# Optimization experiments

Measured on AMD Instinct MI355X. Metric: run time of the kernel, lower is better.

The kernel has to match this reference:

```python
import jax, jax.numpy as jnp
import numpy as np

NUM_INPUTS = 24
FACTOR = 16
VOCAB = 1_000_000
BATCH = 8192
PAIRS = NUM_INPUTS * (NUM_INPUTS - 1) // 2  # 276
HIDDEN = 64


def setup_inputs() -> dict:
    key = jax.random.key(0)
    ks = jax.random.split(key, 8)
    inputs = jax.random.randint(ks[0], (BATCH, NUM_INPUTS), 0, VOCAB)
    s = 0.01
    w = jax.random.normal(ks[1], (VOCAB, 1), dtype=jnp.float32) * s
    v = jax.random.normal(ks[2], (VOCAB, FACTOR), dtype=jnp.float32) * s
    b = jnp.zeros((1,), dtype=jnp.float32)
    W1 = jax.random.normal(ks[3], (PAIRS, 2 * FACTOR, HIDDEN), dtype=jnp.float32) * s
    b1 = jnp.zeros((PAIRS, HIDDEN), dtype=jnp.float32)
    W2 = jax.random.normal(ks[4], (PAIRS, HIDDEN, 1), dtype=jnp.float32) * s
    b2 = jnp.zeros((PAIRS, 1), dtype=jnp.float32)
    return {"inputs": inputs, "w": w, "v": v, "b": b,
            "W1": W1, "b1": b1, "W2": W2, "b2": b2}


def reference(inputs, w, v, b, W1, b1, W2, b2):
    # pair index lists (i < j) -- static
    ii, jj = np.triu_indices(NUM_INPUTS, k=1)
    ii = jnp.asarray(ii)
    jj = jnp.asarray(jj)

    # linear term: sum of 1-dim embeddings over fields
    xw = w[inputs]                      # [B, n, 1]
    l = jnp.sum(xw, axis=(1, 2))        # [B]

    # pairwise concat of factor embeddings
    xv = v[inputs]                      # [B, n, f]
    prods = jnp.concatenate([xv[:, ii, :], xv[:, jj, :]], axis=-1)  # [B, P, 2f]
    prods = jnp.transpose(prods, (1, 0, 2))                         # [P, B, 2f]

    # per-pair stacked MLP: layer 0 relu, layer 1 identity
    h = jax.nn.relu(jnp.einsum('pbi,pio->pbo', prods, W1) + b1[:, None, :])  # [P, B, H]
    out = jnp.einsum('pbi,pio->pbo', h, W2) + b2[:, None, :]                  # [P, B, 1]

    # sum over concat of pair outputs == sum over pairs and last dim
    p = jnp.sum(out, axis=(0, 2))       # [B]

    logits = l + p + b[0]
    return jax.nn.sigmoid(logits)
```

## Files before the change

### kernel.cpp

```cpp
#include <hip/hip_runtime.h>
#include <hip/hip_bf16.h>
#include <math.h>

#define BATCH   8192
#define NFIELD  24
#define FAC     16
#define PAIRS   276
#define HID     64
#define PG      6
#define PPG     (PAIRS / PG)
#define NBB     (BATCH / 64)

typedef __attribute__((ext_vector_type(8))) __bf16 bf16x8;
typedef __attribute__((ext_vector_type(4))) float f32x4;

#define XVT_OFF   0
#define COMBO_OFF 6291456
#define PART_OFF  (COMBO_OFF + 1276416)
#define CONST_OFF (PART_OFF + 196608)

__global__ void prep_embed(const int* __restrict__ inputs,
                           const float* __restrict__ v,
                           __hip_bfloat16* __restrict__ xvT) {
    int t = blockIdx.x * 256 + threadIdx.x;
    int field = t >> 13;
    int b = t & 8191;
    int idx = inputs[b * NFIELD + field];
    const float4* src = (const float4*)(v + (long)idx * FAC);
    union { __hip_bfloat16 h[16]; uint4 u[2]; } tmp;
    float4 a0 = src[0], a1 = src[1], a2 = src[2], a3 = src[3];
    tmp.h[0]  = __float2bfloat16(a0.x); tmp.h[1]  = __float2bfloat16(a0.y);
    tmp.h[2]  = __float2bfloat16(a0.z); tmp.h[3]  = __float2bfloat16(a0.w);
    tmp.h[4]  = __float2bfloat16(a1.x); tmp.h[5]  = __float2bfloat16(a1.y);
    tmp.h[6]  = __float2bfloat16(a1.z); tmp.h[7]  = __float2bfloat16(a1.w);
    tmp.h[8]  = __float2bfloat16(a2.x); tmp.h[9]  = __float2bfloat16(a2.y);
    tmp.h[10] = __float2bfloat16(a2.z); tmp.h[11] = __float2bfloat16(a2.w);
    tmp.h[12] = __float2bfloat16(a3.x); tmp.h[13] = __float2bfloat16(a3.y);
    tmp.h[14] = __float2bfloat16(a3.z); tmp.h[15] = __float2bfloat16(a3.w);
    int bb = b >> 6, row = b & 63;
    __hip_bfloat16* base = xvT + (long)bb * 24576 + field * 1024 + row * 8;
    *(uint4*)base         = tmp.u[0];
    *(uint4*)(base + 512) = tmp.u[1];
}

__global__ void prep_w(const float* __restrict__ W1,
                       const float* __restrict__ W2,
                       const float* __restrict__ b1,
                       const float* __restrict__ b2,
                       const float* __restrict__ bsc,
                       char* __restrict__ combo,
                       float* __restrict__ consts) {
    __shared__ float red[256];
    int t = blockIdx.x * 256 + threadIdx.x;
    int p = t >> 6;
    int L = t & 63;
    int q = L >> 4, c = L & 15;
    char* base = combo + (long)p * 4608;
    union { __hip_bfloat16 h[8]; uint4 u; } buf;
#pragma unroll
    for (int tt = 0; tt < 4; ++tt) {
#pragma unroll
        for (int jj = 0; jj < 8; ++jj)
            buf.h[jj] = __float2bfloat16(W1[p * 2048 + (q * 8 + jj) * 64 + tt * 16 + c]);
        *(uint4*)(base + 512 + tt * 1024 + L * 16) = buf.u;
    }
    if (L < 16) {
        float4 bv = {b1[p * 64 + L], b1[p * 64 + 16 + L], b1[p * 64 + 32 + L], b1[p * 64 + 48 + L]};
        *(float4*)(base + L * 16) = bv;
        float4 wv = {W2[p * 64 + L], W2[p * 64 + 16 + L], W2[p * 64 + 32 + L], W2[p * 64 + 48 + L]};
        *(float4*)(base + 256 + L * 16) = wv;
    }
    if (blockIdx.x == 1) {
        uint4 z = {0, 0, 0, 0};
        for (int k = threadIdx.x; k < 288; k += 256)
            *(uint4*)(combo + (long)PAIRS * 4608 + k * 16) = z;
    }
    if (blockIdx.x == 0) {
        float s = 0.f;
        for (int k = threadIdx.x; k < PAIRS; k += 256) s += b2[k];
        red[threadIdx.x] = s;
        __syncthreads();
        for (int off = 128; off > 0; off >>= 1) {
            if (threadIdx.x < off) red[threadIdx.x] += red[threadIdx.x + off];
            __syncthreads();
        }
        if (threadIdx.x == 0) consts[0] = red[0] + bsc[0];
    }
}

__global__ __launch_bounds__(256, 4) void ffm_main(
        const __hip_bfloat16* __restrict__ xvT,
        const char* __restrict__ combo,
        float* __restrict__ partial) {
    __shared__ __align__(16) __hip_bfloat16 xv_s[24 * 1088];

    int tid  = threadIdx.x;
    int bb   = blockIdx.x & (NBB - 1);
    int pg   = blockIdx.x >> 7;
    int lane = tid & 63;
    int wave = tid >> 6;
    int col  = lane & 15;
    int quad = lane >> 4;

    {
        const uint4* src = (const uint4*)(xvT + (long)bb * 24576);
#pragma unroll
        for (int it = 0; it < 12; ++it) {
            int ch = tid + it * 256;
            *(uint4*)(xv_s + ch * 8 + (ch >> 6) * 32) = src[ch];
        }
    }
    __syncthreads();

    int p0 = pg * PPG;
    int i = 0, rem = p0;
    while (rem >= NFIELD - 1 - i) { rem -= NFIELD - 1 - i; ++i; }
    int j = i + 1 + rem;

    const int arow = (quad & 1) * 544 + (wave * 16 + col) * 8;
    const int mcol = col * 16;
    const char* wp = combo + (long)p0 * 4608;

    float4 mb1 = *(const float4*)(wp + mcol);
    float4 mw2 = *(const float4*)(wp + 256 + mcol);
    bf16x8 f0 = *(const bf16x8*)(wp + 512 + lane * 16);
    bf16x8 f1 = *(const bf16x8*)(wp + 1536 + lane * 16);
    bf16x8 f2 = *(const bf16x8*)(wp + 2560 + lane * 16);
    bf16x8 f3 = *(const bf16x8*)(wp + 3584 + lane * 16);

    float a0 = 0.f, a1 = 0.f, a2 = 0.f, a3 = 0.f;

#pragma unroll 2
    for (int it = 0; it < PPG; ++it) {
        const char* wn = wp + 4608;
        float4 nb1 = *(const float4*)(wn + mcol);
        float4 nw2 = *(const float4*)(wn + 256 + mcol);
        bf16x8 nf0 = *(const bf16x8*)(wn + 512 + lane * 16);
        bf16x8 nf1 = *(const bf16x8*)(wn + 1536 + lane * 16);
        bf16x8 nf2 = *(const bf16x8*)(wn + 2560 + lane * 16);
        bf16x8 nf3 = *(const bf16x8*)(wn + 3584 + lane * 16);

        int fso = (quad < 2) ? i * 1088 : j * 1088;
        bf16x8 af = *(const bf16x8*)(xv_s + fso + arow);

        f32x4 c0 = {mb1.x, mb1.x, mb1.x, mb1.x};
        f32x4 c1 = {mb1.y, mb1.y, mb1.y, mb1.y};
        f32x4 c2 = {mb1.z, mb1.z, mb1.z, mb1.z};
        f32x4 c3 = {mb1.w, mb1.w, mb1.w, mb1.w};
        c0 = __builtin_amdgcn_mfma_f32_16x16x32_bf16(af, f0, c0, 0, 0, 0);
        c1 = __builtin_amdgcn_mfma_f32_16x16x32_bf16(af, f1, c1, 0, 0, 0);
        c2 = __builtin_amdgcn_mfma_f32_16x16x32_bf16(af, f2, c2, 0, 0, 0);
        c3 = __builtin_amdgcn_mfma_f32_16x16x32_bf16(af, f3, c3, 0, 0, 0);

        a0 = fmaf(fmaxf(c0[0], 0.f), mw2.x, a0);
        a1 = fmaf(fmaxf(c0[1], 0.f), mw2.x, a1);
        a2 = fmaf(fmaxf(c0[2], 0.f), mw2.x, a2);
        a3 = fmaf(fmaxf(c0[3], 0.f), mw2.x, a3);
        a0 = fmaf(fmaxf(c1[0], 0.f), mw2.y, a0);
        a1 = fmaf(fmaxf(c1[1], 0.f), mw2.y, a1);
        a2 = fmaf(fmaxf(c1[2], 0.f), mw2.y, a2);
        a3 = fmaf(fmaxf(c1[3], 0.f), mw2.y, a3);
        a0 = fmaf(fmaxf(c2[0], 0.f), mw2.z, a0);
        a1 = fmaf(fmaxf(c2[1], 0.f), mw2.z, a1);
        a2 = fmaf(fmaxf(c2[2], 0.f), mw2.z, a2);
        a3 = fmaf(fmaxf(c2[3], 0.f), mw2.z, a3);
        a0 = fmaf(fmaxf(c3[0], 0.f), mw2.w, a0);
        a1 = fmaf(fmaxf(c3[1], 0.f), mw2.w, a1);
        a2 = fmaf(fmaxf(c3[2], 0.f), mw2.w, a2);
        a3 = fmaf(fmaxf(c3[3], 0.f), mw2.w, a3);

        mb1 = nb1; mw2 = nw2; f0 = nf0; f1 = nf1; f2 = nf2; f3 = nf3;
        wp = wn;
        ++j;
        if (j == NFIELD) { ++i; j = i + 1; }
    }

#pragma unroll
    for (int m = 1; m < 16; m <<= 1) {
        a0 += __shfl_xor(a0, m, 64);
        a1 += __shfl_xor(a1, m, 64);
        a2 += __shfl_xor(a2, m, 64);
        a3 += __shfl_xor(a3, m, 64);
    }
    if (col == 0) {
        f32x4 o; o[0] = a0; o[1] = a1; o[2] = a2; o[3] = a3;
        *(f32x4*)&partial[pg * BATCH + bb * 64 + wave * 16 + quad * 4] = o;
    }
}

__global__ void finalize(const int* __restrict__ inputs,
                         const float* __restrict__ w,
                         const float* __restrict__ consts,
                         const float* __restrict__ partial,
                         float* __restrict__ out) {
    int bidx = blockIdx.x * 256 + threadIdx.x;
    const int4* ip = (const int4*)(inputs + bidx * NFIELD);
    float l = 0.f;
#pragma unroll
    for (int q = 0; q < 6; ++q) {
        int4 v4 = ip[q];
        l += w[v4.x] + w[v4.y] + w[v4.z] + w[v4.w];
    }
    float s = l + consts[0];
#pragma unroll
    for (int g = 0; g < PG; ++g) s += partial[g * BATCH + bidx];
    out[bidx] = 1.0f / (1.0f + expf(-s));
}

extern "C" void kernel_launch(void* const* d_in, const int* in_sizes, int n_in,
                              void* d_out, int out_size, void* d_ws, size_t ws_size,
                              hipStream_t stream) {
    const int*   inputs = (const int*)d_in[0];
    const float* w      = (const float*)d_in[1];
    const float* v      = (const float*)d_in[2];
    const float* bsc    = (const float*)d_in[3];
    const float* W1     = (const float*)d_in[4];
    const float* b1     = (const float*)d_in[5];
    const float* W2     = (const float*)d_in[6];
    const float* b2     = (const float*)d_in[7];
    float* out = (float*)d_out;

    char* ws = (char*)d_ws;
    __hip_bfloat16* xvT = (__hip_bfloat16*)(ws + XVT_OFF);
    char*  combo  = ws + COMBO_OFF;
    float* partial = (float*)(ws + PART_OFF);
    float* consts  = (float*)(ws + CONST_OFF);

    prep_embed<<<BATCH * NFIELD / 256, 256, 0, stream>>>(inputs, v, xvT);
    prep_w<<<PAIRS * 64 / 256, 256, 0, stream>>>(W1, W2, b1, b2, bsc, combo, consts);
    ffm_main<<<NBB * PG, 256, 0, stream>>>(xvT, combo, partial);
    finalize<<<BATCH / 256, 256, 0, stream>>>(inputs, w, consts, partial, out);
}
```

Measured before the change: 157.1 us.

## Merge prep kernels and share LDS embedding tile across two pair groups

The two preprocessing kernels become one launch that splits work by block index, which removes a kernel launch. The main kernel now uses 512-thread blocks in which two halves handle different pair groups over the same staged 64-row embedding tile, halving the global-to-LDS reload of embeddings. The weight prefetch becomes an explicit double-buffered ping-pong of two pair slots, and the zero padding at the end of combo is enlarged so the deeper prefetch does not read past it. More registers per thread and fewer blocks may reduce occupancy and latency hiding.

New measurement: 162.3 us. +3.3%, slower.

```diff
diff --git a/kernel.cpp b/kernel.cpp
--- a/kernel.cpp
+++ b/kernel.cpp
@@ -16,79 +16,122 @@
 
 #define XVT_OFF   0
 #define COMBO_OFF 6291456
-#define PART_OFF  (COMBO_OFF + 1276416)
+#define PART_OFF  (COMBO_OFF + 1281024)
 #define CONST_OFF (PART_OFF + 196608)
 
-__global__ void prep_embed(const int* __restrict__ inputs,
-                           const float* __restrict__ v,
-                           __hip_bfloat16* __restrict__ xvT) {
-    int t = blockIdx.x * 256 + threadIdx.x;
-    int field = t >> 13;
-    int b = t & 8191;
-    int idx = inputs[b * NFIELD + field];
-    const float4* src = (const float4*)(v + (long)idx * FAC);
-    union { __hip_bfloat16 h[16]; uint4 u[2]; } tmp;
-    float4 a0 = src[0], a1 = src[1], a2 = src[2], a3 = src[3];
-    tmp.h[0]  = __float2bfloat16(a0.x); tmp.h[1]  = __float2bfloat16(a0.y);
-    tmp.h[2]  = __float2bfloat16(a0.z); tmp.h[3]  = __float2bfloat16(a0.w);
-    tmp.h[4]  = __float2bfloat16(a1.x); tmp.h[5]  = __float2bfloat16(a1.y);
-    tmp.h[6]  = __float2bfloat16(a1.z); tmp.h[7]  = __float2bfloat16(a1.w);
-    tmp.h[8]  = __float2bfloat16(a2.x); tmp.h[9]  = __float2bfloat16(a2.y);
-    tmp.h[10] = __float2bfloat16(a2.z); tmp.h[11] = __float2bfloat16(a2.w);
-    tmp.h[12] = __float2bfloat16(a3.x); tmp.h[13] = __float2bfloat16(a3.y);
-    tmp.h[14] = __float2bfloat16(a3.z); tmp.h[15] = __float2bfloat16(a3.w);
-    int bb = b >> 6, row = b & 63;
-    __hip_bfloat16* base = xvT + (long)bb * 24576 + field * 1024 + row * 8;
-    *(uint4*)base         = tmp.u[0];
-    *(uint4*)(base + 512) = tmp.u[1];
-}
-
-__global__ void prep_w(const float* __restrict__ W1,
-                       const float* __restrict__ W2,
-                       const float* __restrict__ b1,
-                       const float* __restrict__ b2,
-                       const float* __restrict__ bsc,
-                       char* __restrict__ combo,
-                       float* __restrict__ consts) {
+__global__ void prep_all(const int* __restrict__ inputs,
+                         const float* __restrict__ v,
+                         const float* __restrict__ W1,
+                         const float* __restrict__ W2,
+                         const float* __restrict__ b1,
+                         const float* __restrict__ b2,
+                         const float* __restrict__ bsc,
+                         __hip_bfloat16* __restrict__ xvT,
+                         char* __restrict__ combo,
+                         float* __restrict__ consts) {
     __shared__ float red[256];
-    int t = blockIdx.x * 256 + threadIdx.x;
-    int p = t >> 6;
-    int L = t & 63;
-    int q = L >> 4, c = L & 15;
-    char* base = combo + (long)p * 4608;
-    union { __hip_bfloat16 h[8]; uint4 u; } buf;
-#pragma unroll
-    for (int tt = 0; tt < 4; ++tt) {
-#pragma unroll
-        for (int jj = 0; jj < 8; ++jj)
-            buf.h[jj] = __float2bfloat16(W1[p * 2048 + (q * 8 + jj) * 64 + tt * 16 + c]);
-        *(uint4*)(base + 512 + tt * 1024 + L * 16) = buf.u;
-    }
-    if (L < 16) {
-        float4 bv = {b1[p * 64 + L], b1[p * 64 + 16 + L], b1[p * 64 + 32 + L], b1[p * 64 + 48 + L]};
-        *(float4*)(base + L * 16) = bv;
-        float4 wv = {W2[p * 64 + L], W2[p * 64 + 16 + L], W2[p * 64 + 32 + L], W2[p * 64 + 48 + L]};
-        *(float4*)(base + 256 + L * 16) = wv;
-    }
-    if (blockIdx.x == 1) {
-        uint4 z = {0, 0, 0, 0};
-        for (int k = threadIdx.x; k < 288; k += 256)
-            *(uint4*)(combo + (long)PAIRS * 4608 + k * 16) = z;
-    }
-    if (blockIdx.x == 0) {
-        float s = 0.f;
-        for (int k = threadIdx.x; k < PAIRS; k += 256) s += b2[k];
-        red[threadIdx.x] = s;
-        __syncthreads();
-        for (int off = 128; off > 0; off >>= 1) {
-            if (threadIdx.x < off) red[threadIdx.x] += red[threadIdx.x + off];
+    int blk = blockIdx.x;
+    if (blk < 768) {
+        int t = blk * 256 + threadIdx.x;
+        int field = t >> 13;
+        int b = t & 8191;
+        int idx = inputs[b * NFIELD + field];
+        const float4* src = (const float4*)(v + (long)idx * FAC);
+        union { __hip_bfloat16 h[16]; uint4 u[2]; } tmp;
+        float4 a0 = src[0], a1 = src[1], a2 = src[2], a3 = src[3];
+        tmp.h[0]  = __float2bfloat16(a0.x); tmp.h[1]  = __float2bfloat16(a0.y);
+        tmp.h[2]  = __float2bfloat16(a0.z); tmp.h[3]  = __float2bfloat16(a0.w);
+        tmp.h[4]  = __float2bfloat16(a1.x); tmp.h[5]  = __float2bfloat16(a1.y);
+        tmp.h[6]  = __float2bfloat16(a1.z); tmp.h[7]  = __float2bfloat16(a1.w);
+        tmp.h[8]  = __float2bfloat16(a2.x); tmp.h[9]  = __float2bfloat16(a2.y);
+        tmp.h[10] = __float2bfloat16(a2.z); tmp.h[11] = __float2bfloat16(a2.w);
+        tmp.h[12] = __float2bfloat16(a3.x); tmp.h[13] = __float2bfloat16(a3.y);
+        tmp.h[14] = __float2bfloat16(a3.z); tmp.h[15] = __float2bfloat16(a3.w);
+        int bb = b >> 6, row = b & 63;
+        __hip_bfloat16* base = xvT + (long)bb * 24576 + field * 1024 + row * 8;
+        *(uint4*)base         = tmp.u[0];
+        *(uint4*)(base + 512) = tmp.u[1];
+    } else {
+        int wb = blk - 768;
+        int t = wb * 256 + threadIdx.x;
+        int p = t >> 6;
+        int L = t & 63;
+        int q = L >> 4, c = L & 15;
+        char* base = combo + (long)p * 4608;
+        union { __hip_bfloat16 h[8]; uint4 u; } buf;
+#pragma unroll
+        for (int tt = 0; tt < 4; ++tt) {
+#pragma unroll
+            for (int jj = 0; jj < 8; ++jj)
+                buf.h[jj] = __float2bfloat16(W1[p * 2048 + (q * 8 + jj) * 64 + tt * 16 + c]);
+            *(uint4*)(base + 512 + tt * 1024 + L * 16) = buf.u;
+        }
+        if (L < 16) {
+            float4 bv = {b1[p * 64 + L], b1[p * 64 + 16 + L], b1[p * 64 + 32 + L], b1[p * 64 + 48 + L]};
+            *(float4*)(base + L * 16) = bv;
+            float4 wv = {W2[p * 64 + L], W2[p * 64 + 16 + L], W2[p * 64 + 32 + L], W2[p * 64 + 48 + L]};
+            *(float4*)(base + 256 + L * 16) = wv;
+        }
+        if (wb == 1) {
+            uint4 z = {0, 0, 0, 0};
+            for (int k = threadIdx.x; k < 576; k += 256)
+                *(uint4*)(combo + (long)PAIRS * 4608 + k * 16) = z;
+        }
+        if (wb == 0) {
+            float s = 0.f;
+            for (int k = threadIdx.x; k < PAIRS; k += 256) s += b2[k];
+            red[threadIdx.x] = s;
             __syncthreads();
-        }
-        if (threadIdx.x == 0) consts[0] = red[0] + bsc[0];
-    }
-}
-
-__global__ __launch_bounds__(256, 4) void ffm_main(
+            for (int off = 128; off > 0; off >>= 1) {
+                if (threadIdx.x < off) red[threadIdx.x] += red[threadIdx.x + off];
+                __syncthreads();
+            }
+            if (threadIdx.x == 0) consts[0] = red[0] + bsc[0];
+        }
+    }
+}
+
+#define LOADSET(MB1, MW2, F0, F1, F2, F3, PTR)        \
+    MB1 = *(const float4*)((PTR) + mcol);             \
+    MW2 = *(const float4*)((PTR) + 256 + mcol);       \
+    F0  = *(const bf16x8*)((PTR) + 512  + l16);       \
+    F1  = *(const bf16x8*)((PTR) + 1536 + l16);       \
+    F2  = *(const bf16x8*)((PTR) + 2560 + l16);       \
+    F3  = *(const bf16x8*)((PTR) + 3584 + l16);
+
+#define COMPUTE(MB1, MW2, F0, F1, F2, F3)                                    \
+    {                                                                        \
+        int fso = ((quad < 2) ? i : j) * 1088;                               \
+        bf16x8 af = *(const bf16x8*)(xv_s + fso + arow);                     \
+        f32x4 c0 = {MB1.x, MB1.x, MB1.x, MB1.x};                             \
+        f32x4 c1 = {MB1.y, MB1.y, MB1.y, MB1.y};                             \
+        f32x4 c2 = {MB1.z, MB1.z, MB1.z, MB1.z};                             \
+        f32x4 c3 = {MB1.w, MB1.w, MB1.w, MB1.w};                             \
+        c0 = __builtin_amdgcn_mfma_f32_16x16x32_bf16(af, F0, c0, 0, 0, 0);   \
+        c1 = __builtin_amdgcn_mfma_f32_16x16x32_bf16(af, F1, c1, 0, 0, 0);   \
+        c2 = __builtin_amdgcn_mfma_f32_16x16x32_bf16(af, F2, c2, 0, 0, 0);   \
+        c3 = __builtin_amdgcn_mfma_f32_16x16x32_bf16(af, F3, c3, 0, 0, 0);   \
+        a0 = fmaf(fmaxf(c0[0], 0.f), MW2.x, a0);                             \
+        a1 = fmaf(fmaxf(c0[1], 0.f), MW2.x, a1);                             \
+        a2 = fmaf(fmaxf(c0[2], 0.f), MW2.x, a2);                             \
+        a3 = fmaf(fmaxf(c0[3], 0.f), MW2.x, a3);                             \
+        a0 = fmaf(fmaxf(c1[0], 0.f), MW2.y, a0);                             \
+        a1 = fmaf(fmaxf(c1[1], 0.f), MW2.y, a1);                             \
+        a2 = fmaf(fmaxf(c1[2], 0.f), MW2.y, a2);                             \
+        a3 = fmaf(fmaxf(c1[3], 0.f), MW2.y, a3);                             \
+        a0 = fmaf(fmaxf(c2[0], 0.f), MW2.z, a0);                             \
+        a1 = fmaf(fmaxf(c2[1], 0.f), MW2.z, a1);                             \
+        a2 = fmaf(fmaxf(c2[2], 0.f), MW2.z, a2);                             \
+        a3 = fmaf(fmaxf(c2[3], 0.f), MW2.z, a3);                             \
+        a0 = fmaf(fmaxf(c3[0], 0.f), MW2.w, a0);                             \
+        a1 = fmaf(fmaxf(c3[1], 0.f), MW2.w, a1);                             \
+        a2 = fmaf(fmaxf(c3[2], 0.f), MW2.w, a2);                             \
+        a3 = fmaf(fmaxf(c3[3], 0.f), MW2.w, a3);                             \
+        ++j;                                                                 \
+        if (j == NFIELD) { ++i; j = i + 1; }                                 \
+    }
+
+__global__ __launch_bounds__(512, 4) void ffm_main(
         const __hip_bfloat16* __restrict__ xvT,
         const char* __restrict__ combo,
         float* __restrict__ partial) {
@@ -96,83 +139,48 @@
 
     int tid  = threadIdx.x;
     int bb   = blockIdx.x & (NBB - 1);
-    int pg   = blockIdx.x >> 7;
+    int bkpg = blockIdx.x >> 7;
     int lane = tid & 63;
     int wave = tid >> 6;
     int col  = lane & 15;
     int quad = lane >> 4;
+    int h    = wave >> 2;
+    int r    = wave & 3;
 
     {
         const uint4* src = (const uint4*)(xvT + (long)bb * 24576);
 #pragma unroll
-        for (int it = 0; it < 12; ++it) {
-            int ch = tid + it * 256;
+        for (int it = 0; it < 6; ++it) {
+            int ch = tid + it * 512;
             *(uint4*)(xv_s + ch * 8 + (ch >> 6) * 32) = src[ch];
         }
     }
     __syncthreads();
 
+    int pg = bkpg * 2 + h;
     int p0 = pg * PPG;
     int i = 0, rem = p0;
     while (rem >= NFIELD - 1 - i) { rem -= NFIELD - 1 - i; ++i; }
     int j = i + 1 + rem;
 
-    const int arow = (quad & 1) * 544 + (wave * 16 + col) * 8;
+    const int arow = (quad & 1) * 544 + (r * 16 + col) * 8;
     const int mcol = col * 16;
+    const int l16  = lane * 16;
     const char* wp = combo + (long)p0 * 4608;
 
-    float4 mb1 = *(const float4*)(wp + mcol);
-    float4 mw2 = *(const float4*)(wp + 256 + mcol);
-    bf16x8 f0 = *(const bf16x8*)(wp + 512 + lane * 16);
-    bf16x8 f1 = *(const bf16x8*)(wp + 1536 + lane * 16);
-    bf16x8 f2 = *(const bf16x8*)(wp + 2560 + lane * 16);
-    bf16x8 f3 = *(const bf16x8*)(wp + 3584 + lane * 16);
+    float4 mb1a, mw2a, mb1b, mw2b;
+    bf16x8 fa0, fa1, fa2, fa3, fb0, fb1, fb2, fb3;
+    LOADSET(mb1a, mw2a, fa0, fa1, fa2, fa3, wp)
+    LOADSET(mb1b, mw2b, fb0, fb1, fb2, fb3, wp + 4608)
 
     float a0 = 0.f, a1 = 0.f, a2 = 0.f, a3 = 0.f;
 
-#pragma unroll 2
-    for (int it = 0; it < PPG; ++it) {
-        const char* wn = wp + 4608;
-        float4 nb1 = *(const float4*)(wn + mcol);
-        float4 nw2 = *(const float4*)(wn + 256 + mcol);
-        bf16x8 nf0 = *(const bf16x8*)(wn + 512 + lane * 16);
-        bf16x8 nf1 = *(const bf16x8*)(wn + 1536 + lane * 16);
-        bf16x8 nf2 = *(const bf16x8*)(wn + 2560 + lane * 16);
-        bf16x8 nf3 = *(const bf16x8*)(wn + 3584 + lane * 16);
-
-        int fso = (quad < 2) ? i * 1088 : j * 1088;
-        bf16x8 af = *(const bf16x8*)(xv_s + fso + arow);
-
-        f32x4 c0 = {mb1.x, mb1.x, mb1.x, mb1.x};
-        f32x4 c1 = {mb1.y, mb1.y, mb1.y, mb1.y};
-        f32x4 c2 = {mb1.z, mb1.z, mb1.z, mb1.z};
-        f32x4 c3 = {mb1.w, mb1.w, mb1.w, mb1.w};
-        c0 = __builtin_amdgcn_mfma_f32_16x16x32_bf16(af, f0, c0, 0, 0, 0);
-        c1 = __builtin_amdgcn_mfma_f32_16x16x32_bf16(af, f1, c1, 0, 0, 0);
-        c2 = __builtin_amdgcn_mfma_f32_16x16x32_bf16(af, f2, c2, 0, 0, 0);
-        c3 = __builtin_amdgcn_mfma_f32_16x16x32_bf16(af, f3, c3, 0, 0, 0);
-
-        a0 = fmaf(fmaxf(c0[0], 0.f), mw2.x, a0);
-        a1 = fmaf(fmaxf(c0[1], 0.f), mw2.x, a1);
-        a2 = fmaf(fmaxf(c0[2], 0.f), mw2.x, a2);
-        a3 = fmaf(fmaxf(c0[3], 0.f), mw2.x, a3);
-        a0 = fmaf(fmaxf(c1[0], 0.f), mw2.y, a0);
-        a1 = fmaf(fmaxf(c1[1], 0.f), mw2.y, a1);
-        a2 = fmaf(fmaxf(c1[2], 0.f), mw2.y, a2);
-        a3 = fmaf(fmaxf(c1[3], 0.f), mw2.y, a3);
-        a0 = fmaf(fmaxf(c2[0], 0.f), mw2.z, a0);
-        a1 = fmaf(fmaxf(c2[1], 0.f), mw2.z, a1);
-        a2 = fmaf(fmaxf(c2[2], 0.f), mw2.z, a2);
-        a3 = fmaf(fmaxf(c2[3], 0.f), mw2.z, a3);
-        a0 = fmaf(fmaxf(c3[0], 0.f), mw2.w, a0);
-        a1 = fmaf(fmaxf(c3[1], 0.f), mw2.w, a1);
-        a2 = fmaf(fmaxf(c3[2], 0.f), mw2.w, a2);
-        a3 = fmaf(fmaxf(c3[3], 0.f), mw2.w, a3);
-
-        mb1 = nb1; mw2 = nw2; f0 = nf0; f1 = nf1; f2 = nf2; f3 = nf3;
-        wp = wn;
-        ++j;
-        if (j == NFIELD) { ++i; j = i + 1; }
+    for (int k = 0; k < PPG; k += 2) {
+        COMPUTE(mb1a, mw2a, fa0, fa1, fa2, fa3)
+        LOADSET(mb1a, mw2a, fa0, fa1, fa2, fa3, wp + 2 * 4608)
+        COMPUTE(mb1b, mw2b, fb0, fb1, fb2, fb3)
+        LOADSET(mb1b, mw2b, fb0, fb1, fb2, fb3, wp + 3 * 4608)
+        wp += 2 * 4608;
     }
 
 #pragma unroll
@@ -184,7 +192,7 @@
     }
     if (col == 0) {
         f32x4 o; o[0] = a0; o[1] = a1; o[2] = a2; o[3] = a3;
-        *(f32x4*)&partial[pg * BATCH + bb * 64 + wave * 16 + quad * 4] = o;
+        *(f32x4*)&partial[pg * BATCH + bb * 64 + r * 16 + quad * 4] = o;
     }
 }
 
@@ -222,12 +230,11 @@
 
     char* ws = (char*)d_ws;
     __hip_bfloat16* xvT = (__hip_bfloat16*)(ws + XVT_OFF);
-    char*  combo  = ws + COMBO_OFF;
+    char*  combo   = ws + COMBO_OFF;
     float* partial = (float*)(ws + PART_OFF);
     float* consts  = (float*)(ws + CONST_OFF);
 
-    prep_embed<<<BATCH * NFIELD / 256, 256, 0, stream>>>(inputs, v, xvT);
-    prep_w<<<PAIRS * 64 / 256, 256, 0, stream>>>(W1, W2, b1, b2, bsc, combo, consts);
-    ffm_main<<<NBB * PG, 256, 0, stream>>>(xvT, combo, partial);
+    prep_all<<<768 + 69, 256, 0, stream>>>(inputs, v, W1, W2, b1, b2, bsc, xvT, combo, consts);
+    ffm_main<<<NBB * 3, 512, 0, stream>>>(xvT, combo, partial);
     finalize<<<BATCH / 256, 256, 0, stream>>>(inputs, w, consts, partial, out);
 }
```

## Give each wave a pair set over all 64 rows and merge prep kernels

Applied to the files above, without the earlier changes.

The main kernel now gives each wave its own set of 12 pairs and has it process all 64 batch rows of the tile. Each loaded weight fragment is reused across four MFMA row tiles instead of one, which cuts weight traffic per block. The pair space is split into 24 sets, the last of which does no work, so finalize now sums 24 partials instead of 6, and the partial buffer grows accordingly. The two prep kernels are also merged into a single launch to save one kernel launch. In exchange, each wave holds 16 accumulators, which raises register pressure.

After: 150.3 us. 1.05x faster.

```diff
diff --git a/kernel.cpp b/kernel.cpp
--- a/kernel.cpp
+++ b/kernel.cpp
@@ -7,8 +7,8 @@
 #define FAC     16
 #define PAIRS   276
 #define HID     64
-#define PG      6
-#define PPG     (PAIRS / PG)
+#define NSETS   24
+#define SETLEN  12
 #define NBB     (BATCH / 64)
 
 typedef __attribute__((ext_vector_type(8))) __bf16 bf16x8;
@@ -16,75 +16,78 @@
 
 #define XVT_OFF   0
 #define COMBO_OFF 6291456
-#define PART_OFF  (COMBO_OFF + 1276416)
-#define CONST_OFF (PART_OFF + 196608)
-
-__global__ void prep_embed(const int* __restrict__ inputs,
-                           const float* __restrict__ v,
-                           __hip_bfloat16* __restrict__ xvT) {
-    int t = blockIdx.x * 256 + threadIdx.x;
-    int field = t >> 13;
-    int b = t & 8191;
-    int idx = inputs[b * NFIELD + field];
-    const float4* src = (const float4*)(v + (long)idx * FAC);
-    union { __hip_bfloat16 h[16]; uint4 u[2]; } tmp;
-    float4 a0 = src[0], a1 = src[1], a2 = src[2], a3 = src[3];
-    tmp.h[0]  = __float2bfloat16(a0.x); tmp.h[1]  = __float2bfloat16(a0.y);
-    tmp.h[2]  = __float2bfloat16(a0.z); tmp.h[3]  = __float2bfloat16(a0.w);
-    tmp.h[4]  = __float2bfloat16(a1.x); tmp.h[5]  = __float2bfloat16(a1.y);
-    tmp.h[6]  = __float2bfloat16(a1.z); tmp.h[7]  = __float2bfloat16(a1.w);
-    tmp.h[8]  = __float2bfloat16(a2.x); tmp.h[9]  = __float2bfloat16(a2.y);
-    tmp.h[10] = __float2bfloat16(a2.z); tmp.h[11] = __float2bfloat16(a2.w);
-    tmp.h[12] = __float2bfloat16(a3.x); tmp.h[13] = __float2bfloat16(a3.y);
-    tmp.h[14] = __float2bfloat16(a3.z); tmp.h[15] = __float2bfloat16(a3.w);
-    int bb = b >> 6, row = b & 63;
-    __hip_bfloat16* base = xvT + (long)bb * 24576 + field * 1024 + row * 8;
-    *(uint4*)base         = tmp.u[0];
-    *(uint4*)(base + 512) = tmp.u[1];
-}
-
-__global__ void prep_w(const float* __restrict__ W1,
-                       const float* __restrict__ W2,
-                       const float* __restrict__ b1,
-                       const float* __restrict__ b2,
-                       const float* __restrict__ bsc,
-                       char* __restrict__ combo,
-                       float* __restrict__ consts) {
+#define PART_OFF  (COMBO_OFF + 1285632)
+#define CONST_OFF (PART_OFF + 786432)
+
+__global__ void prep_all(const int* __restrict__ inputs,
+                         const float* __restrict__ v,
+                         const float* __restrict__ W1,
+                         const float* __restrict__ W2,
+                         const float* __restrict__ b1,
+                         const float* __restrict__ b2,
+                         const float* __restrict__ bsc,
+                         __hip_bfloat16* __restrict__ xvT,
+                         char* __restrict__ combo,
+                         float* __restrict__ consts) {
     __shared__ float red[256];
-    int t = blockIdx.x * 256 + threadIdx.x;
-    int p = t >> 6;
-    int L = t & 63;
-    int q = L >> 4, c = L & 15;
-    char* base = combo + (long)p * 4608;
-    union { __hip_bfloat16 h[8]; uint4 u; } buf;
-#pragma unroll
-    for (int tt = 0; tt < 4; ++tt) {
-#pragma unroll
-        for (int jj = 0; jj < 8; ++jj)
-            buf.h[jj] = __float2bfloat16(W1[p * 2048 + (q * 8 + jj) * 64 + tt * 16 + c]);
-        *(uint4*)(base + 512 + tt * 1024 + L * 16) = buf.u;
-    }
-    if (L < 16) {
-        float4 bv = {b1[p * 64 + L], b1[p * 64 + 16 + L], b1[p * 64 + 32 + L], b1[p * 64 + 48 + L]};
-        *(float4*)(base + L * 16) = bv;
-        float4 wv = {W2[p * 64 + L], W2[p * 64 + 16 + L], W2[p * 64 + 32 + L], W2[p * 64 + 48 + L]};
-        *(float4*)(base + 256 + L * 16) = wv;
-    }
-    if (blockIdx.x == 1) {
-        uint4 z = {0, 0, 0, 0};
-        for (int k = threadIdx.x; k < 288; k += 256)
-            *(uint4*)(combo + (long)PAIRS * 4608 + k * 16) = z;
-    }
-    if (blockIdx.x == 0) {
-        float s = 0.f;
-        for (int k = threadIdx.x; k < PAIRS; k += 256) s += b2[k];
-        red[threadIdx.x] = s;
-        __syncthreads();
-        for (int off = 128; off > 0; off >>= 1) {
-            if (threadIdx.x < off) red[threadIdx.x] += red[threadIdx.x + off];
+    int blk = blockIdx.x;
+    if (blk < 768) {
+        int t = blk * 256 + threadIdx.x;
+        int field = t >> 13;
+        int b = t & 8191;
+        int idx = inputs[b * NFIELD + field];
+        const float4* src = (const float4*)(v + (long)idx * FAC);
+        union { __hip_bfloat16 h[16]; uint4 u[2]; } tmp;
+        float4 a0 = src[0], a1 = src[1], a2 = src[2], a3 = src[3];
+        tmp.h[0]  = __float2bfloat16(a0.x); tmp.h[1]  = __float2bfloat16(a0.y);
+        tmp.h[2]  = __float2bfloat16(a0.z); tmp.h[3]  = __float2bfloat16(a0.w);
+        tmp.h[4]  = __float2bfloat16(a1.x); tmp.h[5]  = __float2bfloat16(a1.y);
+        tmp.h[6]  = __float2bfloat16(a1.z); tmp.h[7]  = __float2bfloat16(a1.w);
+        tmp.h[8]  = __float2bfloat16(a2.x); tmp.h[9]  = __float2bfloat16(a2.y);
+        tmp.h[10] = __float2bfloat16(a2.z); tmp.h[11] = __float2bfloat16(a2.w);
+        tmp.h[12] = __float2bfloat16(a3.x); tmp.h[13] = __float2bfloat16(a3.y);
+        tmp.h[14] = __float2bfloat16(a3.z); tmp.h[15] = __float2bfloat16(a3.w);
+        int bb = b >> 6, row = b & 63;
+        __hip_bfloat16* base = xvT + (long)bb * 24576 + field * 1024 + row * 8;
+        *(uint4*)base         = tmp.u[0];
+        *(uint4*)(base + 512) = tmp.u[1];
+    } else {
+        int wb = blk - 768;
+        int t = wb * 256 + threadIdx.x;
+        int p = t >> 6;
+        int L = t & 63;
+        int q = L >> 4, c = L & 15;
+        char* base = combo + (long)p * 4608;
+        union { __hip_bfloat16 h[8]; uint4 u; } buf;
+#pragma unroll
+        for (int tt = 0; tt < 4; ++tt) {
+#pragma unroll
+            for (int jj = 0; jj < 8; ++jj)
+                buf.h[jj] = __float2bfloat16(W1[p * 2048 + (q * 8 + jj) * 64 + tt * 16 + c]);
+            *(uint4*)(base + 512 + tt * 1024 + L * 16) = buf.u;
+        }
+        if (L < 16) {
+            float4 bv = {b1[p * 64 + L], b1[p * 64 + 16 + L], b1[p * 64 + 32 + L], b1[p * 64 + 48 + L]};
+            *(float4*)(base + L * 16) = bv;
+            float4 wv = {W2[p * 64 + L], W2[p * 64 + 16 + L], W2[p * 64 + 32 + L], W2[p * 64 + 48 + L]};
+            *(float4*)(base + 256 + L * 16) = wv;
+        }
+        if (wb == 1) {
+            uint4 z = {0, 0, 0, 0};
+            for (int k = threadIdx.x; k < 864; k += 256)
+                *(uint4*)(combo + (long)PAIRS * 4608 + k * 16) = z;
+        }
+        if (wb == 0) {
+            float s = 0.f;
+            for (int k = threadIdx.x; k < PAIRS; k += 256) s += b2[k];
+            red[threadIdx.x] = s;
             __syncthreads();
-        }
-        if (threadIdx.x == 0) consts[0] = red[0] + bsc[0];
+            for (int off = 128; off > 0; off >>= 1) {
+                if (threadIdx.x < off) red[threadIdx.x] += red[threadIdx.x + off];
+                __syncthreads();
+            }
+            if (threadIdx.x == 0) consts[0] = red[0] + bsc[0];
+        }
     }
 }
 
@@ -112,79 +115,77 @@
     }
     __syncthreads();
 
-    int p0 = pg * PPG;
-    int i = 0, rem = p0;
-    while (rem >= NFIELD - 1 - i) { rem -= NFIELD - 1 - i; ++i; }
-    int j = i + 1 + rem;
-
-    const int arow = (quad & 1) * 544 + (wave * 16 + col) * 8;
-    const int mcol = col * 16;
-    const char* wp = combo + (long)p0 * 4608;
-
-    float4 mb1 = *(const float4*)(wp + mcol);
-    float4 mw2 = *(const float4*)(wp + 256 + mcol);
-    bf16x8 f0 = *(const bf16x8*)(wp + 512 + lane * 16);
-    bf16x8 f1 = *(const bf16x8*)(wp + 1536 + lane * 16);
-    bf16x8 f2 = *(const bf16x8*)(wp + 2560 + lane * 16);
-    bf16x8 f3 = *(const bf16x8*)(wp + 3584 + lane * 16);
-
-    float a0 = 0.f, a1 = 0.f, a2 = 0.f, a3 = 0.f;
+    int ws = pg * 4 + wave;
+    float acc[16];
+#pragma unroll
+    for (int r = 0; r < 16; ++r) acc[r] = 0.f;
+
+    const int abase = (quad & 1) * 544 + col * 8;
+    const int mcol  = col * 16;
+    const int l16   = lane * 16;
+
+    if (ws < 23) {
+        int p0 = ws * SETLEN;
+        int i = 0, rem = p0;
+        while (rem >= NFIELD - 1 - i) { rem -= NFIELD - 1 - i; ++i; }
+        int j = i + 1 + rem;
+
+        const char* wp = combo + (long)p0 * 4608;
+        float4 mb1 = *(const float4*)(wp + mcol);
+        float4 mw2 = *(const float4*)(wp + 256 + mcol);
+        bf16x8 f0 = *(const bf16x8*)(wp + 512 + l16);
+        bf16x8 f1 = *(const bf16x8*)(wp + 1536 + l16);
+        bf16x8 f2 = *(const bf16x8*)(wp + 2560 + l16);
+        bf16x8 f3 = *(const bf16x8*)(wp + 3584 + l16);
 
 #pragma unroll 2
-    for (int it = 0; it < PPG; ++it) {
-        const char* wn = wp + 4608;
-        float4 nb1 = *(const float4*)(wn + mcol);
-        float4 nw2 = *(const float4*)(wn + 256 + mcol);
-        bf16x8 nf0 = *(const bf16x8*)(wn + 512 + lane * 16);
-        bf16x8 nf1 = *(const bf16x8*)(wn + 1536 + lane * 16);
-        bf16x8 nf2 = *(const bf16x8*)(wn + 2560 + lane * 16);
-        bf16x8 nf3 = *(const bf16x8*)(wn + 3584 + lane * 16);
-
-        int fso = (quad < 2) ? i * 1088 : j * 1088;
-        bf16x8 af = *(const bf16x8*)(xv_s + fso + arow);
-
-        f32x4 c0 = {mb1.x, mb1.x, mb1.x, mb1.x};
-        f32x4 c1 = {mb1.y, mb1.y, mb1.y, mb1.y};
-        f32x4 c2 = {mb1.z, mb1.z, mb1.z, mb1.z};
-        f32x4 c3 = {mb1.w, mb1.w, mb1.w, mb1.w};
-        c0 = __builtin_amdgcn_mfma_f32_16x16x32_bf16(af, f0, c0, 0, 0, 0);
-        c1 = __builtin_amdgcn_mfma_f32_16x16x32_bf16(af, f1, c1, 0, 0, 0);
-        c2 = __builtin_amdgcn_mfma_f32_16x16x32_bf16(af, f2, c2, 0, 0, 0);
-        c3 = __builtin_amdgcn_mfma_f32_16x16x32_bf16(af, f3, c3, 0, 0, 0);
-
-        a0 = fmaf(fmaxf(c0[0], 0.f), mw2.x, a0);
-        a1 = fmaf(fmaxf(c0[1], 0.f), mw2.x, a1);
-        a2 = fmaf(fmaxf(c0[2], 0.f), mw2.x, a2);
-        a3 = fmaf(fmaxf(c0[3], 0.f), mw2.x, a3);
-        a0 = fmaf(fmaxf(c1[0], 0.f), mw2.y, a0);
-        a1 = fmaf(fmaxf(c1[1], 0.f), mw2.y, a1);
-        a2 = fmaf(fmaxf(c1[2], 0.f), mw2.y, a2);
-        a3 = fmaf(fmaxf(c1[3], 0.f), mw2.y, a3);
-        a0 = fmaf(fmaxf(c2[0], 0.f), mw2.z, a0);
-        a1 = fmaf(fmaxf(c2[1], 0.f), mw2.z, a1);
-        a2 = fmaf(fmaxf(c2[2], 0.f), mw2.z, a2);
-        a3 = fmaf(fmaxf(c2[3], 0.f), mw2.z, a3);
-        a0 = fmaf(fmaxf(c3[0], 0.f), mw2.w, a0);
-        a1 = fmaf(fmaxf(c3[1], 0.f), mw2.w, a1);
-        a2 = fmaf(fmaxf(c3[2], 0.f), mw2.w, a2);
-        a3 = fmaf(fmaxf(c3[3], 0.f), mw2.w, a3);
-
-        mb1 = nb1; mw2 = nw2; f0 = nf0; f1 = nf1; f2 = nf2; f3 = nf3;
-        wp = wn;
-        ++j;
-        if (j == NFIELD) { ++i; j = i + 1; }
+        for (int k = 0; k < SETLEN; ++k) {
+            const char* wn = wp + 4608;
+            float4 nb1 = *(const float4*)(wn + mcol);
+            float4 nw2 = *(const float4*)(wn + 256 + mcol);
+            bf16x8 nf0 = *(const bf16x8*)(wn + 512 + l16);
+            bf16x8 nf1 = *(const bf16x8*)(wn + 1536 + l16);
+            bf16x8 nf2 = *(const bf16x8*)(wn + 2560 + l16);
+            bf16x8 nf3 = *(const bf16x8*)(wn + 3584 + l16);
+
+            int fso = ((quad < 2) ? i : j) * 1088;
+#pragma unroll
+            for (int t = 0; t < 4; ++t) {
+                bf16x8 af = *(const bf16x8*)(xv_s + fso + abase + t * 128);
+                f32x4 c0 = {mb1.x, mb1.x, mb1.x, mb1.x};
+                f32x4 c1 = {mb1.y, mb1.y, mb1.y, mb1.y};
+                f32x4 c2 = {mb1.z, mb1.z, mb1.z, mb1.z};
+                f32x4 c3 = {mb1.w, mb1.w, mb1.w, mb1.w};
+                c0 = __builtin_amdgcn_mfma_f32_16x16x32_bf16(af, f0, c0, 0, 0, 0);
+                c1 = __builtin_amdgcn_mfma_f32_16x16x32_bf16(af, f1, c1, 0, 0, 0);
+                c2 = __builtin_amdgcn_mfma_f32_16x16x32_bf16(af, f2, c2, 0, 0, 0);
+                c3 = __builtin_amdgcn_mfma_f32_16x16x32_bf16(af, f3, c3, 0, 0, 0);
+#pragma unroll
+                for (int r = 0; r < 4; ++r) {
+                    acc[t * 4 + r] = fmaf(fmaxf(c0[r], 0.f), mw2.x, acc[t * 4 + r]);
+                    acc[t * 4 + r] = fmaf(fmaxf(c1[r], 0.f), mw2.y, acc[t * 4 + r]);
+                    acc[t * 4 + r] = fmaf(fmaxf(c2[r], 0.f), mw2.z, acc[t * 4 + r]);
+                    acc[t * 4 + r] = fmaf(fmaxf(c3[r], 0.f), mw2.w, acc[t * 4 + r]);
+                }
+            }
+            mb1 = nb1; mw2 = nw2; f0 = nf0; f1 = nf1; f2 = nf2; f3 = nf3;
+            wp = wn;
+            ++j;
+            if (j == NFIELD) { ++i; j = i + 1; }
+        }
     }
 
 #pragma unroll
     for (int m = 1; m < 16; m <<= 1) {
-        a0 += __shfl_xor(a0, m, 64);
-        a1 += __shfl_xor(a1, m, 64);
-        a2 += __shfl_xor(a2, m, 64);
-        a3 += __shfl_xor(a3, m, 64);
+#pragma unroll
+        for (int r = 0; r < 16; ++r) acc[r] += __shfl_xor(acc[r], m, 64);
     }
     if (col == 0) {
-        f32x4 o; o[0] = a0; o[1] = a1; o[2] = a2; o[3] = a3;
-        *(f32x4*)&partial[pg * BATCH + bb * 64 + wave * 16 + quad * 4] = o;
+#pragma unroll
+        for (int t = 0; t < 4; ++t) {
+            f32x4 o; o[0] = acc[t*4+0]; o[1] = acc[t*4+1]; o[2] = acc[t*4+2]; o[3] = acc[t*4+3];
+            *(f32x4*)&partial[ws * BATCH + bb * 64 + t * 16 + quad * 4] = o;
+        }
     }
 }
 
@@ -203,7 +204,7 @@
     }
     float s = l + consts[0];
 #pragma unroll
-    for (int g = 0; g < PG; ++g) s += partial[g * BATCH + bidx];
+    for (int g = 0; g < NSETS; ++g) s += partial[g * BATCH + bidx];
     out[bidx] = 1.0f / (1.0f + expf(-s));
 }
 
@@ -222,12 +223,11 @@
 
     char* ws = (char*)d_ws;
     __hip_bfloat16* xvT = (__hip_bfloat16*)(ws + XVT_OFF);
-    char*  combo  = ws + COMBO_OFF;
+    char*  combo   = ws + COMBO_OFF;
     float* partial = (float*)(ws + PART_OFF);
     float* consts  = (float*)(ws + CONST_OFF);
 
-    prep_embed<<<BATCH * NFIELD / 256, 256, 0, stream>>>(inputs, v, xvT);
-    prep_w<<<PAIRS * 64 / 256, 256, 0, stream>>>(W1, W2, b1, b2, bsc, combo, consts);
-    ffm_main<<<NBB * PG, 256, 0, stream>>>(xvT, combo, partial);
+    prep_all<<<768 + 69, 256, 0, stream>>>(inputs, v, W1, W2, b1, b2, bsc, xvT, combo, consts);
+    ffm_main<<<NBB * 6, 256, 0, stream>>>(xvT, combo, partial);
     finalize<<<BATCH / 256, 256, 0, stream>>>(inputs, w, consts, partial, out);
 }
```
